# Optimization experiments

Measured on AMD Instinct MI355X. Metric: run time of the kernel, lower is better.

The kernel has to match this reference:

```python
import jax, jax.numpy as jnp
import numpy as np

LN_EPS = 1e-5


def setup_inputs() -> dict:
    key = jax.random.key(0)
    ks = jax.random.split(key, 16)
    B, T, F = 64, 512, 768
    V, E = 512, 100
    I, H = F + E, 64  # RNN input 868, hidden 64
    s = lambda *sh: 1.0 / np.sqrt(sh[-1])
    return {
        "inputs": jax.random.normal(ks[0], (B, T, F), dtype=jnp.float32),
        "pos": jax.random.randint(ks[1], (B, T), 0, V, dtype=jnp.int64),
        "emb": jax.random.normal(ks[2], (V, E), dtype=jnp.float32),
        # forward-direction RNN params (torch layout: W_ih [H,I], W_hh [H,H])
        "W_ih_f": jax.random.uniform(ks[3], (H, I), jnp.float32, -s(H), s(H)),
        "W_hh_f": jax.random.uniform(ks[4], (H, H), jnp.float32, -s(H), s(H)),
        "b_ih_f": jax.random.uniform(ks[5], (H,), jnp.float32, -s(H), s(H)),
        "b_hh_f": jax.random.uniform(ks[6], (H,), jnp.float32, -s(H), s(H)),
        # reverse direction
        "W_ih_b": jax.random.uniform(ks[7], (H, I), jnp.float32, -s(H), s(H)),
        "W_hh_b": jax.random.uniform(ks[8], (H, H), jnp.float32, -s(H), s(H)),
        "b_ih_b": jax.random.uniform(ks[9], (H,), jnp.float32, -s(H), s(H)),
        "b_hh_b": jax.random.uniform(ks[10], (H,), jnp.float32, -s(H), s(H)),
        # head: Linear(128,32) -> LayerNorm(32) -> ReLU -> Linear(32,4)
        "W1": jax.random.uniform(ks[11], (32, 2 * H), jnp.float32, -s(32, 2 * H), s(32, 2 * H)),
        "b1": jax.random.uniform(ks[12], (32,), jnp.float32, -s(32, 2 * H), s(32, 2 * H)),
        "gamma": jnp.ones((32,), jnp.float32),
        "beta": jnp.zeros((32,), jnp.float32),
        "W2": jax.random.uniform(ks[13], (4, 32), jnp.float32, -s(4, 32), s(4, 32)),
        "b2": jax.random.uniform(ks[14], (4,), jnp.float32, -s(4, 32), s(4, 32)),
    }


def _rnn_scan(xproj, W_hh):
    # xproj: [T, B, H] precomputed input projection (incl. biases)
    B, H = xproj.shape[1], xproj.shape[2]
    h0 = jnp.zeros((B, H), xproj.dtype)

    def step(h, xp_t):
        h = jnp.tanh(xp_t + h @ W_hh.T)
        return h, h

    _, hs = jax.lax.scan(step, h0, xproj)
    return hs  # [T, B, H]


def reference(inputs, pos, emb, W_ih_f, W_hh_f, b_ih_f, b_hh_f,
              W_ih_b, W_hh_b, b_ih_b, b_hh_b, W1, b1, gamma, beta, W2, b2):
    B, T, _ = inputs.shape
    x = jnp.concatenate([inputs, emb[pos]], axis=-1)  # [B, T, 868]
    xt = jnp.transpose(x, (1, 0, 2))  # [T, B, 868]

    # precompute input projections once (the only big GEMMs)
    xp_f = jnp.einsum("tbi,hi->tbh", xt, W_ih_f) + (b_ih_f + b_hh_f)
    xp_b = jnp.einsum("tbi,hi->tbh", xt, W_ih_b) + (b_ih_b + b_hh_b)

    h_f = _rnn_scan(xp_f, W_hh_f)  # [T, B, 64]
    h_b = _rnn_scan(xp_b[::-1], W_hh_b)[::-1]  # reverse direction

    out = jnp.concatenate([h_f, h_b], axis=-1)  # [T, B, 128]
    out = jnp.transpose(out, (1, 0, 2))  # [B, T, 128]

    h = out @ W1.T + b1  # [B, T, 32]
    mu = jnp.mean(h, axis=-1, keepdims=True)
    var = jnp.mean(jnp.square(h - mu), axis=-1, keepdims=True)
    h = (h - mu) * jax.lax.rsqrt(var + LN_EPS) * gamma + beta
    h = jax.nn.relu(h)  # dropout is identity in eval
    return h @ W2.T + b2  # [B, T, 4]
```

## Files before the change

kernel.cpp:

```cpp
#include <hip/hip_runtime.h>

typedef _Float16 half8  __attribute__((ext_vector_type(8)));
typedef _Float16 half2T __attribute__((ext_vector_type(2)));
typedef float    vfloat4 __attribute__((ext_vector_type(4)));

#define T_LEN 512
#define B_SZ  64
#define K_IN  868
#define KP    896
#define E_DIM 100
#define M_TOT (T_LEN * B_SZ)

#define WT_BYTES   (128 * KP * 2)
#define BIAS_OFF   WT_BYTES
#define XP_OFF     (BIAS_OFF + 512)
#define XP_BYTES   ((size_t)M_TOT * 128 * 4)
#define HS_OFF     (XP_OFF + XP_BYTES)

__device__ __forceinline__ void gl_lds16(const void* g, void* l) {
#if __has_builtin(__builtin_amdgcn_global_load_lds)
    __builtin_amdgcn_global_load_lds(
        (const __attribute__((address_space(1))) void*)g,
        (__attribute__((address_space(3))) void*)l, 16, 0, 0);
#else
    *(float4*)l = *(const float4*)g;
#endif
}

__global__ __launch_bounds__(128) void prep_kernel(
    const float* __restrict__ Wf, const float* __restrict__ Wb,
    const float* __restrict__ bif, const float* __restrict__ bhf,
    const float* __restrict__ bib, const float* __restrict__ bhb,
    _Float16* __restrict__ Wt, float* __restrict__ bias)
{
    const int n = blockIdx.y;
    const int k = blockIdx.x * 128 + threadIdx.x;
    float v = 0.f;
    if (k < K_IN) v = (n < 64) ? Wf[n * K_IN + k] : Wb[(n - 64) * K_IN + k];
    Wt[n * KP + k] = (_Float16)v;
    if (blockIdx.x == 0 && threadIdx.x == 0)
        bias[n] = (n < 64) ? (bif[n] + bhf[n]) : (bib[n - 64] + bhb[n - 64]);
}

__global__ __launch_bounds__(256) void gemm_kernel(
    const float* __restrict__ inputs, const int* __restrict__ pos,
    const float* __restrict__ emb, const _Float16* __restrict__ Wt,
    const float* __restrict__ bias, float* __restrict__ xp)
{
    __shared__ float    Ah32[64 * 128];
    __shared__ _Float16 Bh[128 * 128];

    const int tid  = threadIdx.x;
    const int mb   = blockIdx.x;
    const int w    = tid >> 6;
    const int lane = tid & 63;
    const int q    = lane >> 4;
    const int lr   = lane & 15;
    const int rsw  = lr & 7;
    const int wm   = w >> 1;
    const int wn   = w & 1;

    vfloat4 acc[2][4];
#pragma unroll
    for (int i = 0; i < 2; ++i)
#pragma unroll
        for (int j = 0; j < 4; ++j) { vfloat4 z = {0.f, 0.f, 0.f, 0.f}; acc[i][j] = z; }

    const float* Ag = inputs + (size_t)(mb * 64) * 768;

    for (int kc = 0; kc < 7; ++kc) {
        if (kc < 6) {
#pragma unroll
            for (int i = 0; i < 8; ++i) {
                const int slot = (i * 4 + w) * 64 + lane;
                const int row  = slot >> 5;
                const int bp   = slot & 31;
                const int bl   = bp ^ (row & 7);
                gl_lds16(Ag + (size_t)row * 768 + kc * 128 + bl * 4,
                         (char*)Ah32 + slot * 16);
            }
        } else {
#pragma unroll
            for (int it = 0; it < 8; ++it) {
                const int bid = it * 256 + tid;
                const int row = bid >> 5;
                const int bp  = bid & 31;
                const int bl  = bp ^ (row & 7);
                const int p   = pos[mb * 64 + row];
                const float* er = emb + (size_t)p * E_DIM;
                const int c0  = bl * 4;
                float4 v;
                v.x = (c0 + 0 < E_DIM) ? er[c0 + 0] : 0.f;
                v.y = (c0 + 1 < E_DIM) ? er[c0 + 1] : 0.f;
                v.z = (c0 + 2 < E_DIM) ? er[c0 + 2] : 0.f;
                v.w = (c0 + 3 < E_DIM) ? er[c0 + 3] : 0.f;
                *(float4*)((char*)Ah32 + bid * 16) = v;
            }
        }
#pragma unroll
        for (int i = 0; i < 8; ++i) {
            const int slot = (i * 4 + w) * 64 + lane;
            const int row  = slot >> 4;
            const int bp   = slot & 15;
            const int bl   = bp ^ (row & 7);
            gl_lds16(Wt + (size_t)row * KP + kc * 128 + bl * 8,
                     (char*)Bh + slot * 16);
        }
        __syncthreads();

#pragma unroll
        for (int s = 0; s < 4; ++s) {
            const int cbr = (s << 2) | q;
            half8 af[2], bf[4];
#pragma unroll
            for (int mt = 0; mt < 2; ++mt) {
                const int row = wm * 32 + mt * 16 + lr;
                const float* rp = Ah32 + row * 128;
                const vfloat4 lo = *(const vfloat4*)(rp + (((cbr * 2)     ^ rsw) << 2));
                const vfloat4 hi = *(const vfloat4*)(rp + (((cbr * 2 + 1) ^ rsw) << 2));
                half8 a;
                a[0] = (_Float16)lo[0]; a[1] = (_Float16)lo[1];
                a[2] = (_Float16)lo[2]; a[3] = (_Float16)lo[3];
                a[4] = (_Float16)hi[0]; a[5] = (_Float16)hi[1];
                a[6] = (_Float16)hi[2]; a[7] = (_Float16)hi[3];
                af[mt] = a;
            }
#pragma unroll
            for (int nt = 0; nt < 4; ++nt) {
                const int row = wn * 64 + nt * 16 + lr;
                bf[nt] = *(const half8*)&Bh[row * 128 + ((cbr ^ rsw) << 3)];
            }
#pragma unroll
            for (int mt = 0; mt < 2; ++mt)
#pragma unroll
                for (int nt = 0; nt < 4; ++nt)
                    acc[mt][nt] = __builtin_amdgcn_mfma_f32_16x16x32_f16(
                        af[mt], bf[nt], acc[mt][nt], 0, 0, 0);
        }
        __syncthreads();
    }

#pragma unroll
    for (int nt = 0; nt < 4; ++nt) {
        const int n = wn * 64 + nt * 16 + lr;
        const float bv = bias[n];
#pragma unroll
        for (int mt = 0; mt < 2; ++mt) {
#pragma unroll
            for (int r = 0; r < 4; ++r) {
                const int m = mb * 64 + wm * 32 + mt * 16 + q * 4 + r;
                xp[(size_t)m * 128 + n] = acc[mt][nt][r] + bv;
            }
        }
    }
}

#define CHK  32
#define HALO 32

__device__ __forceinline__ float rnn_step(float h, float xcur,
                                          const half2T (&w2)[32])
{
    const float LOG2E2 = 2.885390081777927f;
    const float hn = __builtin_bit_cast(float,
             __builtin_amdgcn_mov_dpp(__builtin_bit_cast(int, h),
                                      0xB1, 0xF, 0xF, false));
    const int hpi = __builtin_bit_cast(int, __builtin_amdgcn_cvt_pkrtz(h, hn));
    float d[4] = {0.f, 0.f, 0.f, 0.f};
#pragma unroll
    for (int i = 0; i < 32; ++i) {
        const int s = __builtin_amdgcn_readlane(hpi, 2 * i);
        d[i & 3] = __builtin_amdgcn_fdot2(__builtin_bit_cast(half2T, s),
                                          w2[i], d[i & 3], false);
    }
    const float z = xcur + ((d[0] + d[1]) + (d[2] + d[3]));
    const float e = __builtin_amdgcn_exp2f(z * LOG2E2);
    const float r = __builtin_amdgcn_rcpf(1.f + e);
    return __builtin_fmaf(-2.f, r, 1.f);
}

__global__ __launch_bounds__(64) void scan_kernel(
    const float* __restrict__ Whf, const float* __restrict__ Whb,
    const float* __restrict__ xp, float* __restrict__ hs)
{
    const int b   = blockIdx.x;
    const int dir = blockIdx.y;
    const int cz  = blockIdx.z;
    const int j   = threadIdx.x;
    const float* Wr = (dir ? Whb : Whf) + j * 64;

    half2T w2[32];
#pragma unroll
    for (int i = 0; i < 32; ++i) {
        w2[i][0] = (_Float16)Wr[2 * i];
        w2[i][1] = (_Float16)Wr[2 * i + 1];
    }

    const size_t base = (size_t)b * T_LEN * 128 + dir * 64 + j;
    const float* xpp = xp + base;
    float*       hsp = hs + base;

    const int fwd = (dir == 0);
    const int stp = fwd ? 1 : -1;
    const int rA0 = cz * CHK,        rA1 = rA0 + CHK - 1;
    const int rB0 = (cz + 8) * CHK,  rB1 = rB0 + CHK - 1;
    int tA = fwd ? (rA0 - HALO) : (rA1 + HALO);
    int tB = fwd ? (rB0 - HALO) : (rB1 + HALO);

    float hA = 0.f, hB = 0.f;

    int tcA = tA < 0 ? 0 : (tA > T_LEN - 1 ? T_LEN - 1 : tA);
    int tcB = tB < 0 ? 0 : (tB > T_LEN - 1 ? T_LEN - 1 : tB);
    float xA = xpp[(size_t)tcA * 128];
    float xB = xpp[(size_t)tcB * 128];
    for (int it = 0; it < HALO; ++it) {
        const int nA = tA + stp, nB = tB + stp;
        const int ncA = nA < 0 ? 0 : (nA > T_LEN - 1 ? T_LEN - 1 : nA);
        const int ncB = nB < 0 ? 0 : (nB > T_LEN - 1 ? T_LEN - 1 : nB);
        const float xnA = xpp[(size_t)ncA * 128];
        const float xnB = xpp[(size_t)ncB * 128];

        const float hA2 = rnn_step(hA, xA, w2);
        const float hB2 = rnn_step(hB, xB, w2);
        hA = ((unsigned)tA < (unsigned)T_LEN) ? hA2 : 0.f;
        hB = ((unsigned)tB < (unsigned)T_LEN) ? hB2 : 0.f;

        xA = xnA; xB = xnB; tA = nA; tB = nB;
    }

    for (int it = 0; it < CHK; ++it) {
        const int nA = tA + stp, nB = tB + stp;
        const int ncA = nA < 0 ? 0 : (nA > T_LEN - 1 ? T_LEN - 1 : nA);
        const int ncB = nB < 0 ? 0 : (nB > T_LEN - 1 ? T_LEN - 1 : nB);
        const float xnA = xpp[(size_t)ncA * 128];
        const float xnB = xpp[(size_t)ncB * 128];

        hA = rnn_step(hA, xA, w2);
        hB = rnn_step(hB, xB, w2);
        hsp[(size_t)tA * 128] = hA;
        hsp[(size_t)tB * 128] = hB;

        xA = xnA; xB = xnB; tA = nA; tB = nB;
    }
}

__global__ __launch_bounds__(256) void head_kernel(
    const float* __restrict__ hs, const float* __restrict__ W1,
    const float* __restrict__ b1, const float* __restrict__ gamma,
    const float* __restrict__ beta, const float* __restrict__ W2,
    const float* __restrict__ b2, float* __restrict__ out)
{
    __shared__ float4 sW1[32 * 32];
    __shared__ float  sb1[32], sg[32], sbt[32], sW2[4 * 34], sb2[4];

    const int t = threadIdx.x;
    const float4* W1v = (const float4*)W1;
    for (int i = t; i < 1024; i += 256) sW1[i] = W1v[i];
    if (t < 32) { sb1[t] = b1[t]; sg[t] = gamma[t]; sbt[t] = beta[t]; }
    if (t < 128) sW2[(t >> 5) * 34 + (t & 31)] = W2[t];
    if (t < 4)  sb2[t] = b2[t];
    __syncthreads();

    const int m  = blockIdx.x * 64 + (t >> 2);
    const int kg = t & 3;

    const float4* xrow = (const float4*)(hs + (size_t)m * 128);
    float4 xq[8];
#pragma unroll
    for (int c = 0; c < 8; ++c) xq[c] = xrow[c * 4 + kg];

    float h1[32];
#pragma unroll
    for (int jj = 0; jj < 32; ++jj) {
        float a = 0.f;
#pragma unroll
        for (int c = 0; c < 8; ++c) {
            const float4 wv = sW1[jj * 32 + c * 4 + kg];
            a += wv.x * xq[c].x + wv.y * xq[c].y + wv.z * xq[c].z + wv.w * xq[c].w;
        }
        a += __builtin_bit_cast(float,
             __builtin_amdgcn_mov_dpp(__builtin_bit_cast(int, a), 0xB1, 0xF, 0xF, false));
        a += __builtin_bit_cast(float,
             __builtin_amdgcn_mov_dpp(__builtin_bit_cast(int, a), 0x4E, 0xF, 0xF, false));
        h1[jj] = a + sb1[jj];
    }

    float mu = 0.f;
#pragma unroll
    for (int jj = 0; jj < 32; ++jj) mu += h1[jj];
    mu *= (1.f / 32.f);
    float var = 0.f;
#pragma unroll
    for (int jj = 0; jj < 32; ++jj) { const float dlt = h1[jj] - mu; var += dlt * dlt; }
    var *= (1.f / 32.f);
    const float rstd = rsqrtf(var + 1e-5f);

    float acc2 = sb2[kg];
#pragma unroll
    for (int jj = 0; jj < 32; ++jj) {
        const float v = (h1[jj] - mu) * rstd * sg[jj] + sbt[jj];
        const float y = v > 0.f ? v : 0.f;
        acc2 += sW2[kg * 34 + jj] * y;
    }
    out[(size_t)m * 4 + kg] = acc2;
}

extern "C" void kernel_launch(void* const* d_in, const int* in_sizes, int n_in,
                              void* d_out, int out_size, void* d_ws, size_t ws_size,
                              hipStream_t stream)
{
    const float* inputs = (const float*)d_in[0];
    const int*   pos    = (const int*)d_in[1];
    const float* emb    = (const float*)d_in[2];
    const float* Wihf   = (const float*)d_in[3];
    const float* Whhf   = (const float*)d_in[4];
    const float* bihf   = (const float*)d_in[5];
    const float* bhhf   = (const float*)d_in[6];
    const float* Wihb   = (const float*)d_in[7];
    const float* Whhb   = (const float*)d_in[8];
    const float* bihb   = (const float*)d_in[9];
    const float* bhhb   = (const float*)d_in[10];
    const float* W1     = (const float*)d_in[11];
    const float* b1v    = (const float*)d_in[12];
    const float* gam    = (const float*)d_in[13];
    const float* bet    = (const float*)d_in[14];
    const float* W2     = (const float*)d_in[15];
    const float* b2v    = (const float*)d_in[16];

    char* ws = (char*)d_ws;
    _Float16* Wt  = (_Float16*)(ws);
    float* bias   = (float*)(ws + BIAS_OFF);
    float* xp     = (float*)(ws + XP_OFF);
    float* hsbuf  = (float*)(ws + HS_OFF);

    prep_kernel<<<dim3(7, 128), 128, 0, stream>>>(Wihf, Wihb, bihf, bhhf, bihb, bhhb, Wt, bias);
    gemm_kernel<<<dim3(512), 256, 0, stream>>>(inputs, pos, emb, Wt, bias, xp);
    scan_kernel<<<dim3(64, 2, 8), 64, 0, stream>>>(Whhf, Whhb, xp, hsbuf);
    head_kernel<<<dim3(512), 256, 0, stream>>>(hsbuf, W1, b1v, gam, bet, W2, b2v, (float*)d_out);
}
```

Baseline: 247.4 us.

## Drop LDS staging in input-projection GEMM; load fragments directly from global memory

```diff
diff --git a/kernel.cpp b/kernel.cpp
--- a/kernel.cpp
+++ b/kernel.cpp
@@ -16,16 +16,6 @@
 #define XP_OFF     (BIAS_OFF + 512)
 #define XP_BYTES   ((size_t)M_TOT * 128 * 4)
 #define HS_OFF     (XP_OFF + XP_BYTES)
-
-__device__ __forceinline__ void gl_lds16(const void* g, void* l) {
-#if __has_builtin(__builtin_amdgcn_global_load_lds)
-    __builtin_amdgcn_global_load_lds(
-        (const __attribute__((address_space(1))) void*)g,
-        (__attribute__((address_space(3))) void*)l, 16, 0, 0);
-#else
-    *(float4*)l = *(const float4*)g;
-#endif
-}
 
 __global__ __launch_bounds__(128) void prep_kernel(
     const float* __restrict__ Wf, const float* __restrict__ Wb,
@@ -42,115 +32,82 @@
         bias[n] = (n < 64) ? (bif[n] + bhf[n]) : (bib[n - 64] + bhb[n - 64]);
 }
 
-__global__ __launch_bounds__(256) void gemm_kernel(
+__global__ __launch_bounds__(128) void gemm_kernel(
     const float* __restrict__ inputs, const int* __restrict__ pos,
     const float* __restrict__ emb, const _Float16* __restrict__ Wt,
     const float* __restrict__ bias, float* __restrict__ xp)
 {
-    __shared__ float    Ah32[64 * 128];
-    __shared__ _Float16 Bh[128 * 128];
-
     const int tid  = threadIdx.x;
-    const int mb   = blockIdx.x;
     const int w    = tid >> 6;
     const int lane = tid & 63;
     const int q    = lane >> 4;
     const int lr   = lane & 15;
-    const int rsw  = lr & 7;
-    const int wm   = w >> 1;
-    const int wn   = w & 1;
-
-    vfloat4 acc[2][4];
+
+    const int r0 = blockIdx.x * 64 + w * 32 + lr;
+
+    const float* aB0 = inputs + (size_t)r0 * 768;
+    const float* aB1 = inputs + (size_t)(r0 + 16) * 768;
+    const float* eB0 = emb + (size_t)pos[r0] * E_DIM;
+    const float* eB1 = emb + (size_t)pos[r0 + 16] * E_DIM;
+    const _Float16* bB = Wt + (size_t)lr * KP + q * 8;
+
+    vfloat4 acc[2][8];
 #pragma unroll
     for (int i = 0; i < 2; ++i)
 #pragma unroll
-        for (int j = 0; j < 4; ++j) { vfloat4 z = {0.f, 0.f, 0.f, 0.f}; acc[i][j] = z; }
-
-    const float* Ag = inputs + (size_t)(mb * 64) * 768;
-
-    for (int kc = 0; kc < 7; ++kc) {
-        if (kc < 6) {
-#pragma unroll
-            for (int i = 0; i < 8; ++i) {
-                const int slot = (i * 4 + w) * 64 + lane;
-                const int row  = slot >> 5;
-                const int bp   = slot & 31;
-                const int bl   = bp ^ (row & 7);
-                gl_lds16(Ag + (size_t)row * 768 + kc * 128 + bl * 4,
-                         (char*)Ah32 + slot * 16);
+        for (int j = 0; j < 8; ++j) { vfloat4 z = {0.f, 0.f, 0.f, 0.f}; acc[i][j] = z; }
+
+    const int qo = q * 8;
+
+#pragma unroll
+    for (int ks = 0; ks < 28; ++ks) {
+        const int k0 = ks * 32;
+
+        half8 a[2];
+#pragma unroll
+        for (int mt = 0; mt < 2; ++mt) {
+            vfloat4 lo, hi;
+            if (ks < 24) {
+                const float* ab = mt ? aB1 : aB0;
+                lo = *(const vfloat4*)(ab + k0 + qo);
+                hi = *(const vfloat4*)(ab + k0 + qo + 4);
+            } else if (ks < 27) {
+                const float* eb = mt ? eB1 : eB0;
+                const int eo = k0 - 768 + qo;
+                lo = *(const vfloat4*)(eb + eo);
+                hi = *(const vfloat4*)(eb + eo + 4);
+            } else {
+                const float* eb = mt ? eB1 : eB0;
+                vfloat4 z = {0.f, 0.f, 0.f, 0.f};
+                lo = (q == 0) ? *(const vfloat4*)(eb + 96) : z;
+                hi = z;
             }
-        } else {
-#pragma unroll
-            for (int it = 0; it < 8; ++it) {
-                const int bid = it * 256 + tid;
-                const int row = bid >> 5;
-                const int bp  = bid & 31;
-                const int bl  = bp ^ (row & 7);
-                const int p   = pos[mb * 64 + row];
-                const float* er = emb + (size_t)p * E_DIM;
-                const int c0  = bl * 4;
-                float4 v;
-                v.x = (c0 + 0 < E_DIM) ? er[c0 + 0] : 0.f;
-                v.y = (c0 + 1 < E_DIM) ? er[c0 + 1] : 0.f;
-                v.z = (c0 + 2 < E_DIM) ? er[c0 + 2] : 0.f;
-                v.w = (c0 + 3 < E_DIM) ? er[c0 + 3] : 0.f;
-                *(float4*)((char*)Ah32 + bid * 16) = v;
-            }
-        }
-#pragma unroll
-        for (int i = 0; i < 8; ++i) {
-            const int slot = (i * 4 + w) * 64 + lane;
-            const int row  = slot >> 4;
-            const int bp   = slot & 15;
-            const int bl   = bp ^ (row & 7);
-            gl_lds16(Wt + (size_t)row * KP + kc * 128 + bl * 8,
-                     (char*)Bh + slot * 16);
-        }
-        __syncthreads();
-
-#pragma unroll
-        for (int s = 0; s < 4; ++s) {
-            const int cbr = (s << 2) | q;
-            half8 af[2], bf[4];
-#pragma unroll
-            for (int mt = 0; mt < 2; ++mt) {
-                const int row = wm * 32 + mt * 16 + lr;
-                const float* rp = Ah32 + row * 128;
-                const vfloat4 lo = *(const vfloat4*)(rp + (((cbr * 2)     ^ rsw) << 2));
-                const vfloat4 hi = *(const vfloat4*)(rp + (((cbr * 2 + 1) ^ rsw) << 2));
-                half8 a;
-                a[0] = (_Float16)lo[0]; a[1] = (_Float16)lo[1];
-                a[2] = (_Float16)lo[2]; a[3] = (_Float16)lo[3];
-                a[4] = (_Float16)hi[0]; a[5] = (_Float16)hi[1];
-                a[6] = (_Float16)hi[2]; a[7] = (_Float16)hi[3];
-                af[mt] = a;
-            }
-#pragma unroll
-            for (int nt = 0; nt < 4; ++nt) {
-                const int row = wn * 64 + nt * 16 + lr;
-                bf[nt] = *(const half8*)&Bh[row * 128 + ((cbr ^ rsw) << 3)];
-            }
-#pragma unroll
-            for (int mt = 0; mt < 2; ++mt)
-#pragma unroll
-                for (int nt = 0; nt < 4; ++nt)
-                    acc[mt][nt] = __builtin_amdgcn_mfma_f32_16x16x32_f16(
-                        af[mt], bf[nt], acc[mt][nt], 0, 0, 0);
-        }
-        __syncthreads();
-    }
-
-#pragma unroll
-    for (int nt = 0; nt < 4; ++nt) {
-        const int n = wn * 64 + nt * 16 + lr;
+            half8 av;
+            av[0] = (_Float16)lo[0]; av[1] = (_Float16)lo[1];
+            av[2] = (_Float16)lo[2]; av[3] = (_Float16)lo[3];
+            av[4] = (_Float16)hi[0]; av[5] = (_Float16)hi[1];
+            av[6] = (_Float16)hi[2]; av[7] = (_Float16)hi[3];
+            a[mt] = av;
+        }
+
+#pragma unroll
+        for (int nt = 0; nt < 8; ++nt) {
+            const half8 bv = *(const half8*)(bB + (size_t)nt * 16 * KP + k0);
+            acc[0][nt] = __builtin_amdgcn_mfma_f32_16x16x32_f16(a[0], bv, acc[0][nt], 0, 0, 0);
+            acc[1][nt] = __builtin_amdgcn_mfma_f32_16x16x32_f16(a[1], bv, acc[1][nt], 0, 0, 0);
+        }
+    }
+
+#pragma unroll
+    for (int nt = 0; nt < 8; ++nt) {
+        const int n = nt * 16 + lr;
         const float bv = bias[n];
 #pragma unroll
         for (int mt = 0; mt < 2; ++mt) {
-#pragma unroll
-            for (int r = 0; r < 4; ++r) {
-                const int m = mb * 64 + wm * 32 + mt * 16 + q * 4 + r;
-                xp[(size_t)m * 128 + n] = acc[mt][nt][r] + bv;
-            }
+            const int mbase = blockIdx.x * 64 + w * 32 + mt * 16 + q * 4;
+#pragma unroll
+            for (int r = 0; r < 4; ++r)
+                xp[(size_t)(mbase + r) * 128 + n] = acc[mt][nt][r] + bv;
         }
     }
 }
@@ -334,7 +291,7 @@
     float* hsbuf  = (float*)(ws + HS_OFF);
 
     prep_kernel<<<dim3(7, 128), 128, 0, stream>>>(Wihf, Wihb, bihf, bhhf, bihb, bhhb, Wt, bias);
-    gemm_kernel<<<dim3(512), 256, 0, stream>>>(inputs, pos, emb, Wt, bias, xp);
+    gemm_kernel<<<dim3(512), 128, 0, stream>>>(inputs, pos, emb, Wt, bias, xp);
     scan_kernel<<<dim3(64, 2, 8), 64, 0, stream>>>(Whhf, Whhb, xp, hsbuf);
     head_kernel<<<dim3(512), 256, 0, stream>>>(hsbuf, W1, b1v, gam, bet, W2, b2v, (float*)d_out);
 }
```

Measured after the change: 271.9 us. +9.9%, slower.
